# Kernel optimization log

Hardware: AMD Instinct MI355X
Metric: run time of the kernel (lower is better)

Reference implementation:

```python
import jax, jax.numpy as jnp
import numpy as np

B, S, D, H = 2, 1024, 1024, 16
DH = D // H


def setup_inputs() -> dict:
    key = jax.random.key(0)
    k1, k2, k3 = jax.random.split(key, 3)
    x = jax.random.normal(k1, (B, S, D), dtype=jnp.float32)
    # nn.Linear weight layout: [out_features, in_features]; scaled for stable softmax logits
    W_qkv = jax.random.normal(k2, (3 * D, D), dtype=jnp.float32) * 0.02
    W_out = jax.random.normal(k3, (D, D), dtype=jnp.float32) * 0.02
    return {"x": x, "W_qkv": W_qkv, "W_out": W_out}


def reference(x, W_qkv, W_out):
    Bx, Sx, Dx = x.shape
    # fused QKV projection: [B,S,3D]
    qkv = jnp.einsum('bsd,ed->bse', x, W_qkv)
    qkv = qkv.reshape(Bx, Sx, 3, H, DH)
    q, k, v = jnp.moveaxis(qkv, 2, 0).transpose(0, 1, 3, 2, 4)
    scale = 1.0 / jnp.sqrt(jnp.asarray(DH, dtype=x.dtype))
    scores = jnp.einsum('bhqd,bhkd->bhqk', q, k) * scale  # [B,H,S,S]
    attn = jax.nn.softmax(scores, axis=-1)
    out = jnp.einsum('bhqk,bhkd->bhqd', attn, v)  # [B,H,S,DH]
    out = out.transpose(0, 2, 1, 3).reshape(Bx, Sx, Dx)  # [B,S,D]
    return jnp.einsum('bsd,ed->bse', out, W_out)
```

## Files before the change

kernel.cpp:

```cpp
#include <hip/hip_runtime.h>

#define B_  2
#define S_  1024
#define D_  1024
#define H_  16
#define DH_ 64

typedef __attribute__((ext_vector_type(8))) short bf16x8;
typedef __attribute__((ext_vector_type(4))) float f32x4;

__device__ __forceinline__ unsigned short f2bf(float f) {
  unsigned int u = __float_as_uint(f);
  u += 0x7fff + ((u >> 16) & 1);
  return (unsigned short)(u >> 16);
}

__device__ __forceinline__ unsigned int pack2bf(float a, float b) {
  return (unsigned int)f2bf(a) | ((unsigned int)f2bf(b) << 16);
}

__device__ __forceinline__ void gload_lds16(const void* g, void* l) {
  __builtin_amdgcn_global_load_lds(
      (const __attribute__((address_space(1))) unsigned int*)g,
      (__attribute__((address_space(3))) unsigned int*)l, 16, 0, 0);
}

__global__ __launch_bounds__(256)
void cvt_kernel(const float4* __restrict__ x, const float4* __restrict__ wq,
                const float4* __restrict__ wo, unsigned short* __restrict__ xb,
                unsigned short* __restrict__ wqb, unsigned short* __restrict__ wob) {
  constexpr int n1 = (B_*S_*D_) / 4;
  constexpr int n2 = (3*D_*D_) / 4;
  constexpr int n3 = (D_*D_) / 4;
  for (int i = blockIdx.x*blockDim.x + threadIdx.x; i < n1+n2+n3;
       i += gridDim.x*blockDim.x) {
    const float4* src; unsigned short* dst; int off;
    if (i < n1)          { src = x;  dst = xb;  off = i; }
    else if (i < n1+n2)  { src = wq; dst = wqb; off = i - n1; }
    else                 { src = wo; dst = wob; off = i - n1 - n2; }
    float4 v = src[off];
    ushort4 r;
    r.x = f2bf(v.x); r.y = f2bf(v.y); r.z = f2bf(v.z); r.w = f2bf(v.w);
    *(ushort4*)&dst[off*4] = r;
  }
}

template<int BM, int M, int N, int K, int EPI>
__global__ __launch_bounds__(256)
void gemm_bt(const unsigned short* __restrict__ A, const unsigned short* __restrict__ Bw,
             float* __restrict__ C, unsigned short* __restrict__ Qb,
             unsigned short* __restrict__ Kb, unsigned short* __restrict__ Vtb) {
  constexpr int NBN = N / 128;
  constexpr int MT  = BM / 32;
  constexpr int AH  = BM / 64;
  __shared__ unsigned short As[BM*32];
  __shared__ unsigned short Bs[128*32];
  const int tid = threadIdx.x;
  const int bid = blockIdx.x;
  const int mb = bid / NBN, nb = bid % NBN;
  const int wid = tid >> 6, lane = tid & 63;
  const int wr = wid >> 1, wc = wid & 1;
  const int lg = lane >> 4, lr = lane & 15;

  f32x4 acc[MT][4] = {};

  const int mrow = mb*BM, nrow = nb*128;
  const int srow = tid >> 2;
  const int scol = (tid & 3) * 8;

  for (int k0 = 0; k0 < K; k0 += 32) {
    #pragma unroll
    for (int h = 0; h < AH; ++h)
      gload_lds16(A  + (size_t)(mrow + h*64 + srow)*K + k0 + scol, &As[(h*256 + tid)*8]);
    #pragma unroll
    for (int h = 0; h < 2; ++h)
      gload_lds16(Bw + (size_t)(nrow + h*64 + srow)*K + k0 + scol, &Bs[(h*256 + tid)*8]);
    __syncthreads();
    bf16x8 af[MT], bfr[4];
    #pragma unroll
    for (int m = 0; m < MT; ++m)
      af[m]  = *(const bf16x8*)&As[(wr*(BM/2) + m*16 + lr)*32 + lg*8];
    #pragma unroll
    for (int n = 0; n < 4; ++n)
      bfr[n] = *(const bf16x8*)&Bs[(wc*64 + n*16 + lr)*32 + lg*8];
    #pragma unroll
    for (int m = 0; m < MT; ++m)
      #pragma unroll
      for (int n = 0; n < 4; ++n)
        acc[m][n] = __builtin_amdgcn_mfma_f32_16x16x32_bf16(af[m], bfr[n], acc[m][n], 0, 0, 0);
    __syncthreads();
  }

  #pragma unroll
  for (int mt = 0; mt < MT; ++mt) {
    const int m0 = mrow + wr*(BM/2) + mt*16 + lg*4;
    #pragma unroll
    for (int nt = 0; nt < 4; ++nt) {
      const int n = nrow + wc*64 + nt*16 + lr;
      f32x4 v = acc[mt][nt];
      if constexpr (EPI == 0) {
        #pragma unroll
        for (int i = 0; i < 4; ++i) C[(size_t)(m0 + i)*N + n] = v[i];
      } else {
        const int t3 = n >> 10, rem = n & 1023;
        const int hh = rem >> 6, dh = rem & 63;
        const int b = m0 >> 10, s0 = m0 & 1023;
        if (t3 == 2) {
          ushort4 pk;
          pk.x = f2bf(v[0]); pk.y = f2bf(v[1]); pk.z = f2bf(v[2]); pk.w = f2bf(v[3]);
          *(ushort4*)&Vtb[(size_t)((b*H_ + hh)*DH_ + dh)*S_ + s0] = pk;
        } else {
          unsigned short* dst = (t3 == 0) ? Qb : Kb;
          #pragma unroll
          for (int i = 0; i < 4; ++i)
            dst[(size_t)((b*H_ + hh)*S_ + s0 + i)*DH_ + dh] = f2bf(v[i]);
        }
      }
    }
  }
}

__global__ __launch_bounds__(256, 2)
void attn_kernel(const unsigned short* __restrict__ Qb, const unsigned short* __restrict__ Kb,
                 const unsigned short* __restrict__ Vtb, unsigned short* __restrict__ AOb) {
  __shared__ unsigned short Ks[2][64*64];
  __shared__ unsigned short Vs[2][64*64];
  __shared__ unsigned short Pl[4][16*72];
  const int bid = blockIdx.x;
  const int xcd = bid & 7, rr = bid >> 3;
  const int qt = rr & 15;
  const int bh = (rr >> 4) * 8 + xcd;
  const int tid = threadIdx.x, wid = tid >> 6, lane = tid & 63;
  const int lg = lane >> 4, lr = lane & 15;
  const unsigned short* Q  = Qb  + (size_t)bh*S_*DH_;
  const unsigned short* Kp = Kb  + (size_t)bh*S_*DH_;
  const unsigned short* Vt = Vtb + (size_t)bh*DH_*S_;
  const int q0 = qt*64 + wid*16;

  bf16x8 qf0 = *(const bf16x8*)&Q[(size_t)(q0 + lr)*DH_ + lg*8];
  bf16x8 qf1 = *(const bf16x8*)&Q[(size_t)(q0 + lr)*DH_ + 32 + lg*8];

  const int sr = tid >> 3;
  const int g0 = (tid & 7) ^ (sr & 7);

  float mrun = -1e30f, lrun = 0.f;
  f32x4 o[4] = {};
  const int rsw = lr & 7;

  gload_lds16(Kp + (size_t)sr*DH_        + g0*8, &Ks[0][tid*8]);
  gload_lds16(Kp + (size_t)(sr+32)*DH_   + g0*8, &Ks[0][(256+tid)*8]);
  gload_lds16(Vt + (size_t)sr*S_         + g0*8, &Vs[0][tid*8]);
  gload_lds16(Vt + (size_t)(sr+32)*S_    + g0*8, &Vs[0][(256+tid)*8]);
  __syncthreads();

  int buf = 0;
  for (int t = 0; t < 16; ++t) {
    const int jn = (t + 1) * 64;
    if (t < 15) {
      gload_lds16(Kp + (size_t)(jn + sr)*DH_      + g0*8, &Ks[buf^1][tid*8]);
      gload_lds16(Kp + (size_t)(jn + sr + 32)*DH_ + g0*8, &Ks[buf^1][(256+tid)*8]);
      gload_lds16(Vt + (size_t)sr*S_      + jn + g0*8,    &Vs[buf^1][tid*8]);
      gload_lds16(Vt + (size_t)(sr+32)*S_ + jn + g0*8,    &Vs[buf^1][(256+tid)*8]);
    }
    f32x4 sv[4];
    __builtin_amdgcn_s_setprio(1);
    #pragma unroll
    for (int f = 0; f < 4; ++f) {
      bf16x8 ka = *(const bf16x8*)&Ks[buf][(16*f + lr)*64 + ((lg     ^ rsw)*8)];
      bf16x8 kb = *(const bf16x8*)&Ks[buf][(16*f + lr)*64 + (((lg+4) ^ rsw)*8)];
      f32x4 z = {};
      z     = __builtin_amdgcn_mfma_f32_16x16x32_bf16(ka, qf0, z, 0, 0, 0);
      sv[f] = __builtin_amdgcn_mfma_f32_16x16x32_bf16(kb, qf1, z, 0, 0, 0);
    }
    __builtin_amdgcn_s_setprio(0);
    float s[16];
    #pragma unroll
    for (int f = 0; f < 4; ++f)
      #pragma unroll
      for (int i = 0; i < 4; ++i) s[4*f + i] = sv[f][i] * 0.125f;
    float t8[8];
    #pragma unroll
    for (int k = 0; k < 8; ++k) t8[k] = fmaxf(s[k], s[k+8]);
    float t4a = fmaxf(t8[0], t8[4]), t4b = fmaxf(t8[1], t8[5]);
    float t4c = fmaxf(t8[2], t8[6]), t4d = fmaxf(t8[3], t8[7]);
    float pmax = fmaxf(fmaxf(t4a, t4b), fmaxf(t4c, t4d));
    pmax = fmaxf(pmax, __shfl_xor(pmax, 16));
    pmax = fmaxf(pmax, __shfl_xor(pmax, 32));
    float mnew = fmaxf(mrun, pmax);
    float cr = __expf(mrun - mnew);
    float p[16];
    #pragma unroll
    for (int k = 0; k < 16; ++k) p[k] = __expf(s[k] - mnew);
    float u8[8];
    #pragma unroll
    for (int k = 0; k < 8; ++k) u8[k] = p[k] + p[k+8];
    float u4a = u8[0]+u8[4], u4b = u8[1]+u8[5], u4c = u8[2]+u8[6], u4d = u8[3]+u8[7];
    float rs = (u4a + u4b) + (u4c + u4d);
    rs += __shfl_xor(rs, 16);
    rs += __shfl_xor(rs, 32);
    lrun = lrun*cr + rs;
    mrun = mnew;
    #pragma unroll
    for (int f = 0; f < 4; ++f) {
      uint2 w;
      w.x = pack2bf(p[4*f],   p[4*f+1]);
      w.y = pack2bf(p[4*f+2], p[4*f+3]);
      *(uint2*)&Pl[wid][lr*72 + f*16 + lg*4] = w;
    }
    #pragma unroll
    for (int dt = 0; dt < 4; ++dt) {
      o[dt][0] *= cr; o[dt][1] *= cr; o[dt][2] *= cr; o[dt][3] *= cr;
    }
    asm volatile("s_waitcnt lgkmcnt(0)" ::: "memory");
    __builtin_amdgcn_s_setprio(1);
    #pragma unroll
    for (int c = 0; c < 2; ++c) {
      bf16x8 pf = *(const bf16x8*)&Pl[wid][lr*72 + c*32 + lg*8];
      #pragma unroll
      for (int dt = 0; dt < 4; ++dt) {
        bf16x8 vfr = *(const bf16x8*)&Vs[buf][(dt*16 + lr)*64 + (((c*4 + lg) ^ rsw)*8)];
        o[dt] = __builtin_amdgcn_mfma_f32_16x16x32_bf16(vfr, pf, o[dt], 0, 0, 0);
      }
    }
    __builtin_amdgcn_s_setprio(0);
    __syncthreads();
    buf ^= 1;
  }

  const float inv = 1.0f / lrun;
  const int b = bh >> 4, hh = bh & 15;
  #pragma unroll
  for (int dt = 0; dt < 4; ++dt) {
    ushort4 pk;
    pk.x = f2bf(o[dt][0]*inv); pk.y = f2bf(o[dt][1]*inv);
    pk.z = f2bf(o[dt][2]*inv); pk.w = f2bf(o[dt][3]*inv);
    *(ushort4*)&AOb[(size_t)(b*S_ + q0 + lr)*D_ + hh*DH_ + dt*16 + lg*4] = pk;
  }
}

extern "C" void kernel_launch(void* const* d_in, const int* in_sizes, int n_in,
                              void* d_out, int out_size, void* d_ws, size_t ws_size,
                              hipStream_t stream) {
  const float* x  = (const float*)d_in[0];
  const float* wq = (const float*)d_in[1];
  const float* wo = (const float*)d_in[2];
  float* out = (float*)d_out;

  unsigned short* w = (unsigned short*)d_ws;
  unsigned short* xb  = w;
  unsigned short* wqb = xb  + 2097152;
  unsigned short* wob = wqb + 3145728;
  unsigned short* qb  = wob + 1048576;
  unsigned short* kb  = qb  + 2097152;
  unsigned short* vtb = kb  + 2097152;
  unsigned short* aob = vtb + 2097152;

  cvt_kernel<<<dim3(1024), dim3(256), 0, stream>>>(
      (const float4*)x, (const float4*)wq, (const float4*)wo, xb, wqb, wob);

  gemm_bt<64, 2048, 3072, 1024, 1><<<dim3(32*24), dim3(256), 0, stream>>>(
      xb, wqb, nullptr, qb, kb, vtb);

  attn_kernel<<<dim3(512), dim3(256), 0, stream>>>(qb, kb, vtb, aob);

  gemm_bt<64, 2048, 1024, 1024, 0><<<dim3(32*8), dim3(256), 0, stream>>>(
      aob, wob, out, nullptr, nullptr, nullptr);
}
```

Before: 141.6 us.

## Triple-buffer LDS loads with prefetch depth two in GEMM and attention

Both the GEMM and attention kernels move from single or double LDS buffering to a three-stage ring with two tiles in flight. Each step now uses one barrier, placed after explicit vmcnt waits, instead of two __syncthreads, so global-to-LDS loads overlap more of the MFMA work. The cost is more shared memory per block, which may lower occupancy. The hand-counted vmcnt values must match the number of loads issued per stage, or the kernels will race.

```diff
diff --git a/kernel.cpp b/kernel.cpp
--- a/kernel.cpp
+++ b/kernel.cpp
@@ -53,8 +53,9 @@
   constexpr int NBN = N / 128;
   constexpr int MT  = BM / 32;
   constexpr int AH  = BM / 64;
-  __shared__ unsigned short As[BM*32];
-  __shared__ unsigned short Bs[128*32];
+  constexpr int NSTEP = K / 32;
+  __shared__ unsigned short As[3][BM*32];
+  __shared__ unsigned short Bs[3][128*32];
   const int tid = threadIdx.x;
   const int bid = blockIdx.x;
   const int mb = bid / NBN, nb = bid % NBN;
@@ -68,27 +69,41 @@
   const int srow = tid >> 2;
   const int scol = (tid & 3) * 8;
 
-  for (int k0 = 0; k0 < K; k0 += 32) {
+  auto STAGE = [&](int t) {
+    const int k0 = t*32, b = t % 3;
     #pragma unroll
     for (int h = 0; h < AH; ++h)
-      gload_lds16(A  + (size_t)(mrow + h*64 + srow)*K + k0 + scol, &As[(h*256 + tid)*8]);
+      gload_lds16(A  + (size_t)(mrow + h*64 + srow)*K + k0 + scol, &As[b][(h*256 + tid)*8]);
     #pragma unroll
     for (int h = 0; h < 2; ++h)
-      gload_lds16(Bw + (size_t)(nrow + h*64 + srow)*K + k0 + scol, &Bs[(h*256 + tid)*8]);
-    __syncthreads();
+      gload_lds16(Bw + (size_t)(nrow + h*64 + srow)*K + k0 + scol, &Bs[b][(h*256 + tid)*8]);
+  };
+
+  STAGE(0);
+  STAGE(1);
+  for (int t = 0; t < NSTEP; ++t) {
+    if (t < NSTEP-1) {
+      if constexpr (AH == 1) asm volatile("s_waitcnt vmcnt(3)" ::: "memory");
+      else                   asm volatile("s_waitcnt vmcnt(4)" ::: "memory");
+    } else {
+      asm volatile("s_waitcnt vmcnt(0)" ::: "memory");
+    }
+    __builtin_amdgcn_s_barrier();
+    __builtin_amdgcn_sched_barrier(0);
+    if (t + 2 < NSTEP) STAGE(t+2);
+    const int b = t % 3;
     bf16x8 af[MT], bfr[4];
     #pragma unroll
     for (int m = 0; m < MT; ++m)
-      af[m]  = *(const bf16x8*)&As[(wr*(BM/2) + m*16 + lr)*32 + lg*8];
+      af[m]  = *(const bf16x8*)&As[b][(wr*(BM/2) + m*16 + lr)*32 + lg*8];
     #pragma unroll
     for (int n = 0; n < 4; ++n)
-      bfr[n] = *(const bf16x8*)&Bs[(wc*64 + n*16 + lr)*32 + lg*8];
+      bfr[n] = *(const bf16x8*)&Bs[b][(wc*64 + n*16 + lr)*32 + lg*8];
     #pragma unroll
     for (int m = 0; m < MT; ++m)
       #pragma unroll
       for (int n = 0; n < 4; ++n)
         acc[m][n] = __builtin_amdgcn_mfma_f32_16x16x32_bf16(af[m], bfr[n], acc[m][n], 0, 0, 0);
-    __syncthreads();
   }
 
   #pragma unroll
@@ -123,8 +138,8 @@
 __global__ __launch_bounds__(256, 2)
 void attn_kernel(const unsigned short* __restrict__ Qb, const unsigned short* __restrict__ Kb,
                  const unsigned short* __restrict__ Vtb, unsigned short* __restrict__ AOb) {
-  __shared__ unsigned short Ks[2][64*64];
-  __shared__ unsigned short Vs[2][64*64];
+  __shared__ unsigned short Ks[3][64*64];
+  __shared__ unsigned short Vs[3][64*64];
   __shared__ unsigned short Pl[4][16*72];
   const int bid = blockIdx.x;
   const int xcd = bid & 7, rr = bid >> 3;
@@ -147,21 +162,23 @@
   f32x4 o[4] = {};
   const int rsw = lr & 7;
 
-  gload_lds16(Kp + (size_t)sr*DH_        + g0*8, &Ks[0][tid*8]);
-  gload_lds16(Kp + (size_t)(sr+32)*DH_   + g0*8, &Ks[0][(256+tid)*8]);
-  gload_lds16(Vt + (size_t)sr*S_         + g0*8, &Vs[0][tid*8]);
-  gload_lds16(Vt + (size_t)(sr+32)*S_    + g0*8, &Vs[0][(256+tid)*8]);
-  __syncthreads();
-
-  int buf = 0;
+  auto STAGE = [&](int t) {
+    const int j = t * 64, b = t % 3;
+    gload_lds16(Kp + (size_t)(j + sr)*DH_      + g0*8, &Ks[b][tid*8]);
+    gload_lds16(Kp + (size_t)(j + sr + 32)*DH_ + g0*8, &Ks[b][(256+tid)*8]);
+    gload_lds16(Vt + (size_t)sr*S_      + j + g0*8,    &Vs[b][tid*8]);
+    gload_lds16(Vt + (size_t)(sr+32)*S_ + j + g0*8,    &Vs[b][(256+tid)*8]);
+  };
+
+  STAGE(0);
+  STAGE(1);
   for (int t = 0; t < 16; ++t) {
-    const int jn = (t + 1) * 64;
-    if (t < 15) {
-      gload_lds16(Kp + (size_t)(jn + sr)*DH_      + g0*8, &Ks[buf^1][tid*8]);
-      gload_lds16(Kp + (size_t)(jn + sr + 32)*DH_ + g0*8, &Ks[buf^1][(256+tid)*8]);
-      gload_lds16(Vt + (size_t)sr*S_      + jn + g0*8,    &Vs[buf^1][tid*8]);
-      gload_lds16(Vt + (size_t)(sr+32)*S_ + jn + g0*8,    &Vs[buf^1][(256+tid)*8]);
-    }
+    if (t < 15) asm volatile("s_waitcnt vmcnt(4)" ::: "memory");
+    else        asm volatile("s_waitcnt vmcnt(0)" ::: "memory");
+    __builtin_amdgcn_s_barrier();
+    __builtin_amdgcn_sched_barrier(0);
+    if (t + 2 < 16) STAGE(t+2);
+    const int buf = t % 3;
     f32x4 sv[4];
     __builtin_amdgcn_s_setprio(1);
     #pragma unroll
@@ -212,6 +229,7 @@
       o[dt][0] *= cr; o[dt][1] *= cr; o[dt][2] *= cr; o[dt][3] *= cr;
     }
     asm volatile("s_waitcnt lgkmcnt(0)" ::: "memory");
+    __builtin_amdgcn_sched_barrier(0);
     __builtin_amdgcn_s_setprio(1);
     #pragma unroll
     for (int c = 0; c < 2; ++c) {
@@ -223,8 +241,6 @@
       }
     }
     __builtin_amdgcn_s_setprio(0);
-    __syncthreads();
-    buf ^= 1;
   }
 
   const float inv = 1.0f / lrun;
```

Result: no change. 140.3 us (-0.9%).
